# Kernel tuning notes

Measured on AMD Instinct MI355X. Metric: run time of the kernel, lower is better.

## Reference

```python
import jax, jax.numpy as jnp
import numpy as np

B, SQ, SK, D, H = 4, 2048, 2048, 1024, 16
HD = D // H


def setup_inputs() -> dict:
    key = jax.random.key(0)
    ks = jax.random.split(key, 8)
    s = 1.0 / np.sqrt(D)
    return {
        "query": jax.random.normal(ks[0], (B, SQ, D), jnp.float32),
        "key_value": jax.random.normal(ks[1], (B, SK, D), jnp.float32),
        "Wq": jax.random.normal(ks[2], (D, D), jnp.float32) * s,
        "bq": jnp.zeros((D,), jnp.float32),
        "Wkv": jax.random.normal(ks[3], (D, 2 * D), jnp.float32) * s,
        "bkv": jnp.zeros((2 * D,), jnp.float32),
        "Wo": jax.random.normal(ks[4], (D, D), jnp.float32) * s,
        "bo": jnp.zeros((D,), jnp.float32),
    }


def reference(query, key_value, Wq, bq, Wkv, bkv, Wo, bo):
    b, sq, _ = query.shape
    sk = key_value.shape[1]
    # Q projection -> [b, H, sq, HD]
    Q = (query @ Wq + bq).reshape(b, sq, H, HD).transpose(0, 2, 1, 3)
    # fused KV projection -> [b, sk, 2, H, HD]
    KV = (key_value @ Wkv + bkv).reshape(b, sk, 2, H, HD)
    K = KV[:, :, 0].transpose(0, 2, 1, 3)  # [b, H, sk, HD]
    V = KV[:, :, 1].transpose(0, 2, 1, 3)
    scale = 1.0 / np.sqrt(HD).astype(np.float32)
    scores = jnp.einsum("bhqd,bhkd->bhqk", Q, K) * scale
    attn = jax.nn.softmax(scores, axis=-1)  # dropout is identity in eval / p=0
    out = jnp.einsum("bhqk,bhkd->bhqd", attn, V)
    out = out.transpose(0, 2, 1, 3).reshape(b, sq, D)
    return out @ Wo + bo
```

## Files before the change

kernel.cpp:

```cpp
#include <hip/hip_runtime.h>
#include <hip/hip_bf16.h>
#include <stdint.h>


typedef __bf16 bf16_t;
typedef __bf16 bf16x8 __attribute__((ext_vector_type(8)));
typedef __bf16 bf16x4 __attribute__((ext_vector_type(4)));
typedef short  s16x4  __attribute__((ext_vector_type(4)));
typedef float  f32x4  __attribute__((ext_vector_type(4)));

#define MFMA16x32(a, b, c) __builtin_amdgcn_mfma_f32_16x16x32_bf16((a), (b), (c), 0, 0, 0)

__device__ __forceinline__ float fast_exp2(float x) {
#if __has_builtin(__builtin_amdgcn_exp2f)
    return __builtin_amdgcn_exp2f(x);
#else
    return exp2f(x);
#endif
}

__device__ __forceinline__ void gload16(const void* g, const void* l) {
    __builtin_amdgcn_global_load_lds(
        (__attribute__((address_space(1))) void*)(uintptr_t)g,
        (__attribute__((address_space(3))) void*)(uintptr_t)l,
        16, 0, 0);
}

#define ATTN_SCALE 0.18033688011112042f

__global__ void prep_kernel(const float* __restrict__ q, const float* __restrict__ kv,
                            const float* __restrict__ Wq, const float* __restrict__ Wkv,
                            const float* __restrict__ Wo, bf16_t* __restrict__ qb,
                            bf16_t* __restrict__ kvb, bf16_t* __restrict__ WqT,
                            bf16_t* __restrict__ WkvT, bf16_t* __restrict__ WoT) {
    __shared__ float tile[64][65];
    int bid = blockIdx.x;
    const int t = threadIdx.x;
    if (bid < 8192) {
        const float* in;
        bf16_t* out;
        if (bid < 4096) { in = q; out = qb; }
        else            { in = kv; out = kvb; bid -= 4096; }
        int i = (bid * 256 + t) * 8;
        const float4* p = (const float4*)(in + i);
        float4 x = p[0], y = p[1];
        bf16x8 v;
        v[0] = (bf16_t)x.x; v[1] = (bf16_t)x.y; v[2] = (bf16_t)x.z; v[3] = (bf16_t)x.w;
        v[4] = (bf16_t)y.x; v[5] = (bf16_t)y.y; v[6] = (bf16_t)y.z; v[7] = (bf16_t)y.w;
        *(bf16x8*)(out + i) = v;
        return;
    }
    bid -= 8192;
    int z = bid >> 9, rem = bid & 511;
    int xb = rem & 31, yb = rem >> 5;
    const float* W;
    bf16_t* WT;
    int N;
    if (z == 0)      { W = Wq;  WT = WqT;  N = 1024; }
    else if (z == 1) { W = Wkv; WT = WkvT; N = 2048; }
    else             { W = Wo;  WT = WoT;  N = 1024; }
    if (xb * 64 >= N) return;
    const int K = 1024;
    const int n0 = xb * 64, k0 = yb * 64;
#pragma unroll
    for (int i = 0; i < 16; ++i) {
        int idx = i * 256 + t;
        int r = idx >> 6, c = idx & 63;
        tile[r][c] = W[(size_t)(k0 + r) * N + n0 + c];
    }
    __syncthreads();
#pragma unroll
    for (int i = 0; i < 16; ++i) {
        int idx = i * 256 + t;
        int r = idx >> 6, c = idx & 63;
        WT[(size_t)(n0 + r) * K + k0 + c] = (bf16_t)tile[c][r];
    }
}

__global__ __launch_bounds__(256, 3)
void gemm_qkv(const bf16_t* __restrict__ qb, const bf16_t* __restrict__ kvb,
              const bf16_t* __restrict__ WqT, const bf16_t* __restrict__ WkvT,
              const float* __restrict__ bq, const float* __restrict__ bkv,
              bf16_t* __restrict__ Qp, bf16_t* __restrict__ Kb,
              bf16_t* __restrict__ Vt) {
    __shared__ __align__(16) char pool[16384 + 4 * 64 * 72 * 2];
    bf16_t* sA = (bf16_t*)pool;
    bf16_t* sB = (bf16_t*)(pool + 8192);

    const int tid  = threadIdx.x;
    const int lane = tid & 63, w = tid >> 6;
    const int wr = w >> 1, wc = w & 1;
    const int quad = lane >> 4, l15 = lane & 15;
    const int x3 = l15 & 3;
    const bool isQ = blockIdx.x < 8;
    const bf16_t* A    = isQ ? qb : kvb;
    const bf16_t* BT   = isQ ? WqT : WkvT;
    const float*  bias = isQ ? bq : bkv;
    const int row0 = blockIdx.y * 128;
    const int col0 = (isQ ? blockIdx.x : (blockIdx.x - 8)) * 128;
    const int K = 1024;

    f32x4 acc[4][4];
    const f32x4 fz = {0.f, 0.f, 0.f, 0.f};
#pragma unroll
    for (int m = 0; m < 4; ++m)
#pragma unroll
        for (int n = 0; n < 4; ++n) acc[m][n] = fz;

    for (int kt = 0; kt < K; kt += 32) {
#pragma unroll
        for (int i = 0; i < 2; ++i) {
            int c = i * 256 + tid;
            int r = c >> 2, cr = c & 3;
            int g = cr ^ (r & 3);
            gload16(A + (size_t)(row0 + r) * K + kt + g * 8,
                    (const char*)sA + i * 4096 + w * 1024);
            gload16(BT + (size_t)(col0 + r) * K + kt + g * 8,
                    (const char*)sB + i * 4096 + w * 1024);
        }
        __syncthreads();

        bf16x8 af[4], bfr[4];
#pragma unroll
        for (int m = 0; m < 4; ++m)
            af[m] = *(const bf16x8*)(sA + (wr * 64 + m * 16 + l15) * 32 + (quad ^ x3) * 8);
#pragma unroll
        for (int n = 0; n < 4; ++n)
            bfr[n] = *(const bf16x8*)(sB + (wc * 64 + n * 16 + l15) * 32 + (quad ^ x3) * 8);
#pragma unroll
        for (int m = 0; m < 4; ++m)
#pragma unroll
            for (int n = 0; n < 4; ++n)
                acc[m][n] = MFMA16x32(af[m], bfr[n], acc[m][n]);
        __syncthreads();
    }

    if (!isQ && col0 >= 1024) {
        bf16_t* sT = (bf16_t*)(pool + 16384) + w * (64 * 72);
        const int j0  = col0 - 1024 + wc * 64;
        const int hh  = j0 >> 6;
        const int sk0 = row0 + wr * 64;
        const int bb  = sk0 >> 11;
        const int skl = sk0 & 2047;
#pragma unroll
        for (int n = 0; n < 4; ++n) {
            int hd = n * 16 + l15;
            float bv = bkv[1024 + j0 + n * 16 + l15];
#pragma unroll
            for (int m = 0; m < 4; ++m) {
                bf16x4 v4;
                v4[0] = (bf16_t)(acc[m][n][0] + bv);
                v4[1] = (bf16_t)(acc[m][n][1] + bv);
                v4[2] = (bf16_t)(acc[m][n][2] + bv);
                v4[3] = (bf16_t)(acc[m][n][3] + bv);
                *(bf16x4*)(sT + hd * 72 + (m >> 1) * 32 + quad * 8 + (m & 1) * 4) = v4;
            }
        }
        bf16_t* vdst = Vt + (((size_t)(bb * 16 + hh) * 64) << 11) + skl;
#pragma unroll
        for (int it = 0; it < 8; ++it) {
            int hd = it * 8 + (lane >> 3);
            int sc = (lane & 7) * 8;
            bf16x8 v = *(const bf16x8*)(sT + hd * 72 + sc);
            *(bf16x8*)(vdst + ((size_t)hd << 11) + sc) = v;
        }
        return;
    }

#pragma unroll
    for (int m = 0; m < 4; ++m) {
        int rg_base = row0 + wr * 64 + m * 16 + quad * 4;
#pragma unroll
        for (int n = 0; n < 4; ++n) {
            int cg = col0 + wc * 64 + n * 16 + l15;
            float bv = bias[cg];
#pragma unroll
            for (int r = 0; r < 4; ++r) {
                int rg = rg_base + r;
                float v = acc[m][n][r] + bv;
                int bb = rg >> 11, sr = rg & 2047;
                int hh = cg >> 6, hd = cg & 63;
                size_t idx = (((size_t)(bb * 16 + hh) * 2048 + sr) << 6) | hd;
                if (isQ) Qp[idx] = (bf16_t)(v * ATTN_SCALE);
                else     Kb[idx] = (bf16_t)v;
            }
        }
    }
}

__global__ __launch_bounds__(256, 3)
void gemm_out(const bf16_t* __restrict__ A, const bf16_t* __restrict__ BT,
              const float* __restrict__ bias, float* __restrict__ out,
              int M, int N, int K) {
    __shared__ __align__(16) bf16_t sA[128 * 32];
    __shared__ __align__(16) bf16_t sB[128 * 32];
    const int tid  = threadIdx.x;
    const int lane = tid & 63, w = tid >> 6;
    const int wr = w >> 1, wc = w & 1;
    const int quad = lane >> 4, l15 = lane & 15;
    const int x3 = l15 & 3;
    const int row0 = blockIdx.y * 128, col0 = blockIdx.x * 128;

    f32x4 acc[4][4];
    const f32x4 fz = {0.f, 0.f, 0.f, 0.f};
#pragma unroll
    for (int m = 0; m < 4; ++m)
#pragma unroll
        for (int n = 0; n < 4; ++n) acc[m][n] = fz;

    for (int kt = 0; kt < K; kt += 32) {
#pragma unroll
        for (int i = 0; i < 2; ++i) {
            int c = i * 256 + tid;
            int r = c >> 2, cr = c & 3;
            int g = cr ^ (r & 3);
            gload16(A + (size_t)(row0 + r) * K + kt + g * 8,
                    (const char*)sA + i * 4096 + w * 1024);
            gload16(BT + (size_t)(col0 + r) * K + kt + g * 8,
                    (const char*)sB + i * 4096 + w * 1024);
        }
        __syncthreads();

        bf16x8 af[4], bfr[4];
#pragma unroll
        for (int m = 0; m < 4; ++m)
            af[m] = *(const bf16x8*)(sA + (wr * 64 + m * 16 + l15) * 32 + (quad ^ x3) * 8);
#pragma unroll
        for (int n = 0; n < 4; ++n)
            bfr[n] = *(const bf16x8*)(sB + (wc * 64 + n * 16 + l15) * 32 + (quad ^ x3) * 8);
#pragma unroll
        for (int m = 0; m < 4; ++m)
#pragma unroll
            for (int n = 0; n < 4; ++n)
                acc[m][n] = MFMA16x32(af[m], bfr[n], acc[m][n]);
        __syncthreads();
    }

#pragma unroll
    for (int m = 0; m < 4; ++m) {
        int rg_base = row0 + wr * 64 + m * 16 + quad * 4;
#pragma unroll
        for (int n = 0; n < 4; ++n) {
            int cg = col0 + wc * 64 + n * 16 + l15;
            float bv = bias[cg];
#pragma unroll
            for (int r = 0; r < 4; ++r)
                out[(size_t)(rg_base + r) * N + cg] = acc[m][n][r] + bv;
        }
    }
}

__global__ __launch_bounds__(256, 5)
void attn_kernel(const bf16_t* __restrict__ Qp, const bf16_t* __restrict__ Kb,
                 const bf16_t* __restrict__ Vt, bf16_t* __restrict__ Ob) {
    __shared__ __align__(16) char pool[32768];
    bf16_t* sQ   = (bf16_t*)pool;
    float*  redO = (float*)pool;
    float*  redL = (float*)(pool + 16384);

    const int tid = threadIdx.x;
    const int lane = tid & 63, w = tid >> 6;
    const int wq = w >> 1, wk = w & 1;
    const int quad = lane >> 4, l15 = lane & 15;
    const int x7 = l15 & 7;
    const int bhid = blockIdx.x & 63;
    const int qt   = blockIdx.x >> 6;
    const int b = bhid >> 4, h = bhid & 15;
    const size_t bh = (size_t)bhid;

    const bf16_t* Qg = Qp + bh * (2048 * 64) + (size_t)qt * (64 * 64);
    const bf16_t* Kg = Kb + bh * (2048 * 64);
    const bf16_t* Vg = Vt + bh * (64 * 2048);

    const int srow = tid >> 3;
    const int sg   = (tid & 7) ^ (srow & 7);

#pragma unroll
    for (int hh = 0; hh < 2; ++hh) {
        int row = hh * 32 + srow;
        gload16(Qg + (size_t)row * 64 + sg * 8, pool + hh * 4096 + w * 1024);
        gload16(Kg + (size_t)row * 64 + sg * 8, pool + 8192 + hh * 4096 + w * 1024);
        gload16(Vg + (size_t)row * 2048 + sg * 8, pool + 24576 + hh * 4096 + w * 1024);
    }
    __syncthreads();

    bf16x8 qf[2][2];
#pragma unroll
    for (int qb = 0; qb < 2; ++qb)
#pragma unroll
        for (int hh = 0; hh < 2; ++hh)
            qf[qb][hh] = *(const bf16x8*)(sQ + (wq * 32 + qb * 16 + l15) * 64 +
                                          ((hh * 4 + quad) ^ x7) * 8);
    __syncthreads();

    const f32x4 fz = {0.f, 0.f, 0.f, 0.f};
    bf16x8 ones8;
#pragma unroll
    for (int i = 0; i < 8; ++i) ones8[i] = (bf16_t)1.f;

    f32x4 o_[2][4];
    f32x4 lacc[2];
#pragma unroll
    for (int qb = 0; qb < 2; ++qb) {
        lacc[qb] = fz;
#pragma unroll
        for (int nh = 0; nh < 4; ++nh) o_[qb][nh] = fz;
    }

    const int vslot = ((wk * 4 + quad) ^ x7) * 8;

    for (int t = 0; t < 32; ++t) {
        if (t < 31) {
            const bf16_t* Kt = Kg + (size_t)(t + 1) * (64 * 64);
            char* kb_ = pool + 8192 + (((t + 1) & 1) << 13);
            char* vb_ = ((t + 1) & 1) ? pool : pool + 24576;
#pragma unroll
            for (int hh = 0; hh < 2; ++hh) {
                int row = hh * 32 + srow;
                gload16(Kt + (size_t)row * 64 + sg * 8, kb_ + hh * 4096 + w * 1024);
                gload16(Vg + (size_t)row * 2048 + (t + 1) * 64 + sg * 8,
                        vb_ + hh * 4096 + w * 1024);
            }
        }
        const bf16_t* k0 = (const bf16_t*)(pool + 8192 + ((t & 1) << 13));
        const bf16_t* v0 = (const bf16_t*)((t & 1) ? pool : pool + 24576);

        bf16x8 kf0[2], kf1[2], vf[4];
#pragma unroll
        for (int kg = 0; kg < 2; ++kg) {
            const bf16_t* krow = k0 + (wk * 32 + kg * 16 + l15) * 64;
            kf0[kg] = *(const bf16x8*)(krow + (quad ^ x7) * 8);
            kf1[kg] = *(const bf16x8*)(krow + ((quad + 4) ^ x7) * 8);
        }
#pragma unroll
        for (int nh = 0; nh < 4; ++nh)
            vf[nh] = *(const bf16x8*)(v0 + (nh * 16 + l15) * 64 + vslot);

        f32x4 s_[2][2];
#pragma unroll
        for (int kg = 0; kg < 2; ++kg)
#pragma unroll
            for (int qb = 0; qb < 2; ++qb) {
                s_[kg][qb] = MFMA16x32(kf0[kg], qf[qb][0], fz);
                s_[kg][qb] = MFMA16x32(kf1[kg], qf[qb][1], s_[kg][qb]);
            }

        bf16x8 pf8[2];
#pragma unroll
        for (int qb = 0; qb < 2; ++qb) {
#pragma unroll
            for (int kg = 0; kg < 2; ++kg)
#pragma unroll
                for (int r = 0; r < 4; ++r)
                    pf8[qb][kg * 4 + r] = (bf16_t)fast_exp2(s_[kg][qb][r]);
            lacc[qb] = MFMA16x32(pf8[qb], ones8, lacc[qb]);
        }

#pragma unroll
        for (int nh = 0; nh < 4; ++nh)
#pragma unroll
            for (int qb = 0; qb < 2; ++qb)
                o_[qb][nh] = MFMA16x32(pf8[qb], vf[nh], o_[qb][nh]);
        __syncthreads();
    }

    if (l15 == 0) {
#pragma unroll
        for (int qb = 0; qb < 2; ++qb)
#pragma unroll
            for (int r = 0; r < 4; ++r)
                redL[w * 32 + qb * 16 + quad * 4 + r] = lacc[qb][r];
    }

    const int cq  = tid >> 2;
    const int cwq = cq >> 5, cql = cq & 31;
    const int chb = (tid & 3) * 8;
    const size_t orow = (size_t)b * 2048 + (size_t)qt * 64 + cq;

#pragma unroll
    for (int ph = 0; ph < 2; ++ph) {
        __syncthreads();
#pragma unroll
        for (int qb = 0; qb < 2; ++qb)
#pragma unroll
            for (int nj = 0; nj < 2; ++nj) {
                int nh = ph * 2 + nj;
#pragma unroll
                for (int r = 0; r < 4; ++r)
                    redO[w * 1024 + (qb * 16 + quad * 4 + r) * 32 + nj * 16 + l15] =
                        o_[qb][nh][r];
            }
        __syncthreads();

        float lt = redL[cwq * 64 + cql] + redL[cwq * 64 + 32 + cql];
        float linv = 1.f / lt;
        float4 a0 = {0, 0, 0, 0}, a1 = {0, 0, 0, 0};
#pragma unroll
        for (int wk2 = 0; wk2 < 2; ++wk2) {
            const float4* p = (const float4*)(redO + (cwq * 2 + wk2) * 1024 + cql * 32 + chb);
            float4 x = p[0], y = p[1];
            a0.x += x.x; a0.y += x.y; a0.z += x.z; a0.w += x.w;
            a1.x += y.x; a1.y += y.y; a1.z += y.z; a1.w += y.w;
        }
        bf16x8 ov;
        ov[0] = (bf16_t)(a0.x * linv); ov[1] = (bf16_t)(a0.y * linv);
        ov[2] = (bf16_t)(a0.z * linv); ov[3] = (bf16_t)(a0.w * linv);
        ov[4] = (bf16_t)(a1.x * linv); ov[5] = (bf16_t)(a1.y * linv);
        ov[6] = (bf16_t)(a1.z * linv); ov[7] = (bf16_t)(a1.w * linv);
        *(bf16x8*)(Ob + orow * 1024 + h * 64 + ph * 32 + chb) = ov;
    }
}

extern "C" void kernel_launch(void* const* d_in, const int* in_sizes, int n_in,
                              void* d_out, int out_size, void* d_ws, size_t ws_size,
                              hipStream_t stream) {
    const float* query     = (const float*)d_in[0];
    const float* key_value = (const float*)d_in[1];
    const float* Wq  = (const float*)d_in[2];
    const float* bq  = (const float*)d_in[3];
    const float* Wkv = (const float*)d_in[4];
    const float* bkv = (const float*)d_in[5];
    const float* Wo  = (const float*)d_in[6];
    const float* bo  = (const float*)d_in[7];
    float* out = (float*)d_out;

    char* ws = (char*)d_ws;
    const size_t MB = 1024 * 1024;
    bf16_t* WqT  = (bf16_t*)(ws + 0 * MB);
    bf16_t* WkvT = (bf16_t*)(ws + 2 * MB);
    bf16_t* WoT  = (bf16_t*)(ws + 6 * MB);
    bf16_t* qb   = (bf16_t*)(ws + 8 * MB);
    bf16_t* kvb  = (bf16_t*)(ws + 24 * MB);
    bf16_t* Qp   = (bf16_t*)(ws + 40 * MB);
    bf16_t* Kb   = (bf16_t*)(ws + 56 * MB);
    bf16_t* Vt   = (bf16_t*)(ws + 72 * MB);
    bf16_t* Ob   = (bf16_t*)(ws + 88 * MB);

    prep_kernel<<<9728, 256, 0, stream>>>(query, key_value, Wq, Wkv, Wo,
                                          qb, kvb, WqT, WkvT, WoT);
    gemm_qkv<<<dim3(24, 64), 256, 0, stream>>>(qb, kvb, WqT, WkvT, bq, bkv,
                                               Qp, Kb, Vt);
    attn_kernel<<<2048, 256, 0, stream>>>(Qp, Kb, Vt, Ob);
    gemm_out<<<dim3(8, 64), 256, 0, stream>>>(Ob, WoT, bo, out, 8192, 1024, 1024);
}
```

Before: 300.5 us.

## Load V fragments directly from global into registers, double-buffered

V tiles are no longer staged through LDS. Each lane loads its V MFMA operand fragments straight from global memory into registers, double-buffered across two unrolled iterations. This shrinks the LDS pool from 32KB to 24KB, removes one post-Q-load barrier, and drops the LDS reads for V. The launch-bounds occupancy hint is lowered from 5 to 4 to leave room for the extra registers. The trade-off is uncoalesced 16-byte global loads (stride of 2048 elements per lane row) and higher register pressure.

```diff
diff --git a/kernel.cpp b/kernel.cpp
--- a/kernel.cpp
+++ b/kernel.cpp
@@ -250,10 +250,10 @@
     }
 }
 
-__global__ __launch_bounds__(256, 5)
+__global__ __launch_bounds__(256, 4)
 void attn_kernel(const bf16_t* __restrict__ Qp, const bf16_t* __restrict__ Kb,
                  const bf16_t* __restrict__ Vt, bf16_t* __restrict__ Ob) {
-    __shared__ __align__(16) char pool[32768];
+    __shared__ __align__(16) char pool[24576];
     bf16_t* sQ   = (bf16_t*)pool;
     float*  redO = (float*)pool;
     float*  redL = (float*)(pool + 16384);
@@ -280,8 +280,14 @@
         int row = hh * 32 + srow;
         gload16(Qg + (size_t)row * 64 + sg * 8, pool + hh * 4096 + w * 1024);
         gload16(Kg + (size_t)row * 64 + sg * 8, pool + 8192 + hh * 4096 + w * 1024);
-        gload16(Vg + (size_t)row * 2048 + sg * 8, pool + 24576 + hh * 4096 + w * 1024);
-    }
+    }
+
+    const bf16_t* vbase = Vg + (size_t)l15 * 2048 + wk * 32 + quad * 8;
+    bf16x8 vA[4], vB[4];
+#pragma unroll
+    for (int nh = 0; nh < 4; ++nh)
+        vA[nh] = *(const bf16x8*)(vbase + (size_t)nh * 32768);
+
     __syncthreads();
 
     bf16x8 qf[2][2];
@@ -291,7 +297,6 @@
         for (int hh = 0; hh < 2; ++hh)
             qf[qb][hh] = *(const bf16x8*)(sQ + (wq * 32 + qb * 16 + l15) * 64 +
                                           ((hh * 4 + quad) ^ x7) * 8);
-    __syncthreads();
 
     const f32x4 fz = {0.f, 0.f, 0.f, 0.f};
     bf16x8 ones8;
@@ -307,62 +312,60 @@
         for (int nh = 0; nh < 4; ++nh) o_[qb][nh] = fz;
     }
 
-    const int vslot = ((wk * 4 + quad) ^ x7) * 8;
-
-    for (int t = 0; t < 32; ++t) {
-        if (t < 31) {
-            const bf16_t* Kt = Kg + (size_t)(t + 1) * (64 * 64);
-            char* kb_ = pool + 8192 + (((t + 1) & 1) << 13);
-            char* vb_ = ((t + 1) & 1) ? pool : pool + 24576;
-#pragma unroll
-            for (int hh = 0; hh < 2; ++hh) {
-                int row = hh * 32 + srow;
-                gload16(Kt + (size_t)row * 64 + sg * 8, kb_ + hh * 4096 + w * 1024);
-                gload16(Vg + (size_t)row * 2048 + (t + 1) * 64 + sg * 8,
-                        vb_ + hh * 4096 + w * 1024);
-            }
-        }
-        const bf16_t* k0 = (const bf16_t*)(pool + 8192 + ((t & 1) << 13));
-        const bf16_t* v0 = (const bf16_t*)((t & 1) ? pool : pool + 24576);
-
-        bf16x8 kf0[2], kf1[2], vf[4];
-#pragma unroll
-        for (int kg = 0; kg < 2; ++kg) {
-            const bf16_t* krow = k0 + (wk * 32 + kg * 16 + l15) * 64;
-            kf0[kg] = *(const bf16x8*)(krow + (quad ^ x7) * 8);
-            kf1[kg] = *(const bf16x8*)(krow + ((quad + 4) ^ x7) * 8);
-        }
-#pragma unroll
-        for (int nh = 0; nh < 4; ++nh)
-            vf[nh] = *(const bf16x8*)(v0 + (nh * 16 + l15) * 64 + vslot);
-
-        f32x4 s_[2][2];
-#pragma unroll
-        for (int kg = 0; kg < 2; ++kg)
-#pragma unroll
-            for (int qb = 0; qb < 2; ++qb) {
-                s_[kg][qb] = MFMA16x32(kf0[kg], qf[qb][0], fz);
-                s_[kg][qb] = MFMA16x32(kf1[kg], qf[qb][1], s_[kg][qb]);
-            }
-
-        bf16x8 pf8[2];
-#pragma unroll
-        for (int qb = 0; qb < 2; ++qb) {
-#pragma unroll
-            for (int kg = 0; kg < 2; ++kg)
-#pragma unroll
-                for (int r = 0; r < 4; ++r)
-                    pf8[qb][kg * 4 + r] = (bf16_t)fast_exp2(s_[kg][qb][r]);
-            lacc[qb] = MFMA16x32(pf8[qb], ones8, lacc[qb]);
-        }
-
-#pragma unroll
-        for (int nh = 0; nh < 4; ++nh)
-#pragma unroll
-            for (int qb = 0; qb < 2; ++qb)
-                o_[qb][nh] = MFMA16x32(pf8[qb], vf[nh], o_[qb][nh]);
-        __syncthreads();
-    }
+#define ATTN_TILE(T, VC, VN)                                                     \
+    {                                                                            \
+        const int t_ = (T);                                                      \
+        if (t_ < 31) {                                                           \
+            const bf16_t* Kt = Kg + (size_t)(t_ + 1) * (64 * 64);                \
+            char* kb_ = pool + 8192 + (((t_ + 1) & 1) << 13);                    \
+            _Pragma("unroll")                                                    \
+            for (int hh = 0; hh < 2; ++hh) {                                     \
+                int row = hh * 32 + srow;                                        \
+                gload16(Kt + (size_t)row * 64 + sg * 8, kb_ + hh * 4096 + w * 1024); \
+            }                                                                    \
+            _Pragma("unroll")                                                    \
+            for (int nh = 0; nh < 4; ++nh)                                       \
+                VN[nh] = *(const bf16x8*)(vbase + (size_t)nh * 32768 + (t_ + 1) * 64); \
+        }                                                                        \
+        const bf16_t* k0 = (const bf16_t*)(pool + 8192 + ((t_ & 1) << 13));      \
+        bf16x8 kf0[2], kf1[2];                                                   \
+        _Pragma("unroll")                                                        \
+        for (int kg = 0; kg < 2; ++kg) {                                         \
+            const bf16_t* krow = k0 + (wk * 32 + kg * 16 + l15) * 64;            \
+            kf0[kg] = *(const bf16x8*)(krow + (quad ^ x7) * 8);                  \
+            kf1[kg] = *(const bf16x8*)(krow + ((quad + 4) ^ x7) * 8);            \
+        }                                                                        \
+        f32x4 s_[2][2];                                                          \
+        _Pragma("unroll")                                                        \
+        for (int kg = 0; kg < 2; ++kg)                                           \
+            _Pragma("unroll")                                                    \
+            for (int qb = 0; qb < 2; ++qb) {                                     \
+                s_[kg][qb] = MFMA16x32(kf0[kg], qf[qb][0], fz);                  \
+                s_[kg][qb] = MFMA16x32(kf1[kg], qf[qb][1], s_[kg][qb]);          \
+            }                                                                    \
+        bf16x8 pf8[2];                                                           \
+        _Pragma("unroll")                                                        \
+        for (int qb = 0; qb < 2; ++qb) {                                         \
+            _Pragma("unroll")                                                    \
+            for (int kg = 0; kg < 2; ++kg)                                       \
+                _Pragma("unroll")                                                \
+                for (int r = 0; r < 4; ++r)                                      \
+                    pf8[qb][kg * 4 + r] = (bf16_t)fast_exp2(s_[kg][qb][r]);      \
+            lacc[qb] = MFMA16x32(pf8[qb], ones8, lacc[qb]);                      \
+        }                                                                        \
+        _Pragma("unroll")                                                        \
+        for (int nh = 0; nh < 4; ++nh)                                           \
+            _Pragma("unroll")                                                    \
+            for (int qb = 0; qb < 2; ++qb)                                       \
+                o_[qb][nh] = MFMA16x32(pf8[qb], VC[nh], o_[qb][nh]);             \
+        __syncthreads();                                                         \
+    }
+
+    for (int tt = 0; tt < 16; ++tt) {
+        ATTN_TILE(2 * tt,     vA, vB)
+        ATTN_TILE(2 * tt + 1, vB, vA)
+    }
+#undef ATTN_TILE
 
     if (l15 == 0) {
 #pragma unroll
```

New measurement: 378.7 us. 1.26x slower.

## Store V in MFMA-fragment order and load it straight to registers

Applied to the files above, without the earlier changes.

The QKV GEMM epilogue now writes V directly in a pre-swizzled per-lane fragment layout, so each lane's bf16x8 operand is contiguous. This removes the LDS transpose buffer from the GEMM. In the attention kernel, V fragments are loaded from global memory into registers instead of being staged through shared memory, which shrinks LDS use and removes one barrier. The V loads are no longer prefetched a tile ahead, so their global latency is exposed inside the loop, and the launch-bounds occupancy hint drops from 5 to 4.

```diff
diff --git a/kernel.cpp b/kernel.cpp
--- a/kernel.cpp
+++ b/kernel.cpp
@@ -83,7 +83,7 @@
               const float* __restrict__ bq, const float* __restrict__ bkv,
               bf16_t* __restrict__ Qp, bf16_t* __restrict__ Kb,
               bf16_t* __restrict__ Vt) {
-    __shared__ __align__(16) char pool[16384 + 4 * 64 * 72 * 2];
+    __shared__ __align__(16) char pool[16384];
     bf16_t* sA = (bf16_t*)pool;
     bf16_t* sB = (bf16_t*)(pool + 8192);
 
@@ -136,34 +136,26 @@
     }
 
     if (!isQ && col0 >= 1024) {
-        bf16_t* sT = (bf16_t*)(pool + 16384) + w * (64 * 72);
         const int j0  = col0 - 1024 + wc * 64;
         const int hh  = j0 >> 6;
         const int sk0 = row0 + wr * 64;
         const int bb  = sk0 >> 11;
-        const int skl = sk0 & 2047;
-#pragma unroll
-        for (int n = 0; n < 4; ++n) {
-            int hd = n * 16 + l15;
-            float bv = bkv[1024 + j0 + n * 16 + l15];
-#pragma unroll
-            for (int m = 0; m < 4; ++m) {
-                bf16x4 v4;
-                v4[0] = (bf16_t)(acc[m][n][0] + bv);
-                v4[1] = (bf16_t)(acc[m][n][1] + bv);
-                v4[2] = (bf16_t)(acc[m][n][2] + bv);
-                v4[3] = (bf16_t)(acc[m][n][3] + bv);
-                *(bf16x4*)(sT + hd * 72 + (m >> 1) * 32 + quad * 8 + (m & 1) * 4) = v4;
+        const int tt  = (sk0 & 2047) >> 6;
+        bf16_t* vdst = Vt + ((((size_t)(bb * 16 + hh) * 32 + tt) * 2) * 4) * 512 +
+                       (size_t)lane * 8;
+#pragma unroll
+        for (int wkh = 0; wkh < 2; ++wkh)
+#pragma unroll
+            for (int n = 0; n < 4; ++n) {
+                float bv = bkv[1024 + j0 + n * 16 + l15];
+                bf16x8 v8;
+#pragma unroll
+                for (int r = 0; r < 4; ++r) {
+                    v8[r]     = (bf16_t)(acc[2 * wkh][n][r] + bv);
+                    v8[4 + r] = (bf16_t)(acc[2 * wkh + 1][n][r] + bv);
+                }
+                *(bf16x8*)(vdst + ((size_t)wkh * 4 + n) * 512) = v8;
             }
-        }
-        bf16_t* vdst = Vt + (((size_t)(bb * 16 + hh) * 64) << 11) + skl;
-#pragma unroll
-        for (int it = 0; it < 8; ++it) {
-            int hd = it * 8 + (lane >> 3);
-            int sc = (lane & 7) * 8;
-            bf16x8 v = *(const bf16x8*)(sT + hd * 72 + sc);
-            *(bf16x8*)(vdst + ((size_t)hd << 11) + sc) = v;
-        }
         return;
     }
 
@@ -250,10 +242,10 @@
     }
 }
 
-__global__ __launch_bounds__(256, 5)
+__global__ __launch_bounds__(256, 4)
 void attn_kernel(const bf16_t* __restrict__ Qp, const bf16_t* __restrict__ Kb,
                  const bf16_t* __restrict__ Vt, bf16_t* __restrict__ Ob) {
-    __shared__ __align__(16) char pool[32768];
+    __shared__ __align__(16) char pool[24576];
     bf16_t* sQ   = (bf16_t*)pool;
     float*  redO = (float*)pool;
     float*  redL = (float*)(pool + 16384);
@@ -270,7 +262,7 @@
 
     const bf16_t* Qg = Qp + bh * (2048 * 64) + (size_t)qt * (64 * 64);
     const bf16_t* Kg = Kb + bh * (2048 * 64);
-    const bf16_t* Vg = Vt + bh * (64 * 2048);
+    const bf16_t* vtile = Vt + bh * 131072 + (size_t)wk * 2048 + (size_t)lane * 8;
 
     const int srow = tid >> 3;
     const int sg   = (tid & 7) ^ (srow & 7);
@@ -280,7 +272,6 @@
         int row = hh * 32 + srow;
         gload16(Qg + (size_t)row * 64 + sg * 8, pool + hh * 4096 + w * 1024);
         gload16(Kg + (size_t)row * 64 + sg * 8, pool + 8192 + hh * 4096 + w * 1024);
-        gload16(Vg + (size_t)row * 2048 + sg * 8, pool + 24576 + hh * 4096 + w * 1024);
     }
     __syncthreads();
 
@@ -291,7 +282,6 @@
         for (int hh = 0; hh < 2; ++hh)
             qf[qb][hh] = *(const bf16x8*)(sQ + (wq * 32 + qb * 16 + l15) * 64 +
                                           ((hh * 4 + quad) ^ x7) * 8);
-    __syncthreads();
 
     const f32x4 fz = {0.f, 0.f, 0.f, 0.f};
     bf16x8 ones8;
@@ -306,35 +296,32 @@
 #pragma unroll
         for (int nh = 0; nh < 4; ++nh) o_[qb][nh] = fz;
     }
-
-    const int vslot = ((wk * 4 + quad) ^ x7) * 8;
 
     for (int t = 0; t < 32; ++t) {
         if (t < 31) {
             const bf16_t* Kt = Kg + (size_t)(t + 1) * (64 * 64);
             char* kb_ = pool + 8192 + (((t + 1) & 1) << 13);
-            char* vb_ = ((t + 1) & 1) ? pool : pool + 24576;
 #pragma unroll
             for (int hh = 0; hh < 2; ++hh) {
                 int row = hh * 32 + srow;
                 gload16(Kt + (size_t)row * 64 + sg * 8, kb_ + hh * 4096 + w * 1024);
-                gload16(Vg + (size_t)row * 2048 + (t + 1) * 64 + sg * 8,
-                        vb_ + hh * 4096 + w * 1024);
             }
         }
+
+        bf16x8 vf[4];
+#pragma unroll
+        for (int nh = 0; nh < 4; ++nh)
+            vf[nh] = *(const bf16x8*)(vtile + (size_t)t * 4096 + nh * 512);
+
         const bf16_t* k0 = (const bf16_t*)(pool + 8192 + ((t & 1) << 13));
-        const bf16_t* v0 = (const bf16_t*)((t & 1) ? pool : pool + 24576);
-
-        bf16x8 kf0[2], kf1[2], vf[4];
+
+        bf16x8 kf0[2], kf1[2];
 #pragma unroll
         for (int kg = 0; kg < 2; ++kg) {
             const bf16_t* krow = k0 + (wk * 32 + kg * 16 + l15) * 64;
             kf0[kg] = *(const bf16x8*)(krow + (quad ^ x7) * 8);
             kf1[kg] = *(const bf16x8*)(krow + ((quad + 4) ^ x7) * 8);
         }
-#pragma unroll
-        for (int nh = 0; nh < 4; ++nh)
-            vf[nh] = *(const bf16x8*)(v0 + (nh * 16 + l15) * 64 + vslot);
 
         f32x4 s_[2][2];
 #pragma unroll
@@ -361,6 +348,7 @@
 #pragma unroll
             for (int qb = 0; qb < 2; ++qb)
                 o_[qb][nh] = MFMA16x32(pf8[qb], vf[nh], o_[qb][nh]);
+
         __syncthreads();
     }
 
```

Result: no change. 305.5 us (+1.6%).
